# Kernel optimization log

Measured on AMD Instinct MI355X. Metric: run time of the kernel, lower is better.

Reference implementation:

```python
import jax, jax.numpy as jnp
import numpy as np

B, Q, K, D, H = 8, 128, 1024, 256, 256


def setup_inputs() -> dict:
    key = jax.random.key(0)
    ks = jax.random.split(key, 7)
    queries = jax.random.normal(ks[0], (B, Q, D), dtype=jnp.float32)
    keys = jax.random.normal(ks[1], (B, K, D), dtype=jnp.float32)
    values = jax.random.normal(ks[2], (B, K, D), dtype=jnp.float32)
    W_q = jax.random.normal(ks[3], (H, D), dtype=jnp.float32) * (1.0 / np.sqrt(D))
    W_k = jax.random.normal(ks[4], (H, D), dtype=jnp.float32) * (1.0 / np.sqrt(D))
    w_v = jax.random.normal(ks[5], (H,), dtype=jnp.float32) * (1.0 / np.sqrt(H))
    valid_lens = jax.random.randint(ks[6], (B,), 0, K, dtype=jnp.int64)
    return {"queries": queries, "keys": keys, "values": values,
            "W_q": W_q, "W_k": W_k, "w_v": w_v, "valid_lens": valid_lens}


def reference(queries, keys, values, W_q, W_k, w_v, valid_lens):
    # Linear projections (bias=False): [B,Q,H], [B,K,H]
    q = jnp.einsum("bqd,hd->bqh", queries, W_q)
    k = jnp.einsum("bkd,hd->bkh", keys, W_k)
    # Broadcast add -> tanh -> reduce with w_v: scores [B,Q,K]
    features = jnp.tanh(q[:, :, None, :] + k[:, None, :, :])  # [B,Q,K,H]
    scores = jnp.einsum("bqkh,h->bqk", features, w_v)
    # Masked softmax over K: positions >= valid_len get -1e9
    mask = jnp.arange(K)[None, None, :] < valid_lens[:, None, None]
    scores = jnp.where(mask, scores, jnp.float32(-1e9))
    attn = jax.nn.softmax(scores, axis=-1)  # [B,Q,K]
    # Dropout p=0.0 (eval): identity. bmm(attn, values) -> [B,Q,Dv]
    return jnp.einsum("bqk,bkv->bqv", attn, values)
```

## Files before the change

kernel.cpp:

```cpp
#include <hip/hip_runtime.h>

#define BB 8
#define QQ 128
#define KK 1024
#define DD 256
#define HH 256

#define KSPLIT 8
#define KCH (KK / KSPLIT)
#define QT 8

#define TWO_LOG2E     2.8853900817779268f
#define NEG_TWO_LOG2E -2.8853900817779268f

__global__ __launch_bounds__(256) void proj_kernel(const float* __restrict__ queries,
                                                   const float* __restrict__ keys,
                                                   const float* __restrict__ Wq,
                                                   const float* __restrict__ Wk,
                                                   float* __restrict__ eproj) {
    __shared__ float As[64][68];
    __shared__ float Ws[64][68];
    const int t  = threadIdx.x;
    const int tr = t & 15;
    const int th = t >> 4;
    const int r0 = blockIdx.x * 64;
    const int h0 = blockIdx.y * 64;
    const bool isQ = (r0 < BB * QQ);
    const float* A = isQ ? (queries + (size_t)r0 * DD)
                         : (keys + (size_t)(r0 - BB * QQ) * DD);
    const float* W = isQ ? Wq : Wk;

    float acc[4][4] = {};

    for (int dc = 0; dc < DD; dc += 64) {
#pragma unroll
        for (int i = 0; i < 4; ++i) {
            int fi  = t + 256 * i;
            int row = fi >> 4;
            int c4  = (fi & 15) << 2;
            *(float4*)&As[row][c4] = *(const float4*)&A[(size_t)row * DD + dc + c4];
            *(float4*)&Ws[row][c4] = *(const float4*)&W[(size_t)(h0 + row) * DD + dc + c4];
        }
        __syncthreads();
#pragma unroll 4
        for (int dd = 0; dd < 64; dd += 4) {
            float4 a4[4], w4[4];
#pragma unroll
            for (int i = 0; i < 4; ++i) a4[i] = *(float4*)&As[tr + 16 * i][dd];
#pragma unroll
            for (int i = 0; i < 4; ++i) w4[i] = *(float4*)&Ws[th + 16 * i][dd];
#pragma unroll
            for (int ri = 0; ri < 4; ++ri)
#pragma unroll
                for (int hi = 0; hi < 4; ++hi) {
                    acc[ri][hi] += a4[ri].x * w4[hi].x + a4[ri].y * w4[hi].y +
                                   a4[ri].z * w4[hi].z + a4[ri].w * w4[hi].w;
                }
        }
        __syncthreads();
    }
#pragma unroll
    for (int ri = 0; ri < 4; ++ri)
#pragma unroll
        for (int hi = 0; hi < 4; ++hi) {
            eproj[(size_t)(r0 + tr + 16 * ri) * HH + h0 + th + 16 * hi] =
                __builtin_amdgcn_exp2f(TWO_LOG2E * acc[ri][hi]);
        }
}

__global__ __launch_bounds__(256) void score_kernel(const float* __restrict__ eproj,
                                                    const float* __restrict__ wv,
                                                    const int* __restrict__ vlen,
                                                    float* __restrict__ p) {
    __shared__ float qs[32][68];
    __shared__ float ks_[64][68];
    const int t  = threadIdx.x;
    const int tk = t & 15;
    const int tq = t >> 4;
    const int b  = blockIdx.z;
    const int q0 = blockIdx.y * 32;
    const int k0 = blockIdx.x * 64;

    const float* qpB = eproj + ((size_t)(b * QQ + q0)) * HH;
    const float* kpB = eproj + ((size_t)(BB * QQ + b * KK + k0)) * HH;

    float acc[2][4] = {};

    for (int hc = 0; hc < HH; hc += 64) {
#pragma unroll
        for (int i = 0; i < 2; ++i) {
            int fi = t + 256 * i; int row = fi >> 4; int c4 = (fi & 15) << 2;
            *(float4*)&qs[row][c4] = *(const float4*)&qpB[(size_t)row * HH + hc + c4];
        }
#pragma unroll
        for (int i = 0; i < 4; ++i) {
            int fi = t + 256 * i; int row = fi >> 4; int c4 = (fi & 15) << 2;
            *(float4*)&ks_[row][c4] = *(const float4*)&kpB[(size_t)row * HH + hc + c4];
        }
        __syncthreads();

#pragma unroll 4
        for (int hh = 0; hh < 64; hh += 4) {
            const float4 w4 = *(const float4*)&wv[hc + hh];
            const float* wa = (const float*)&w4;
            float4 q4[2], k4[4];
            q4[0] = *(float4*)&qs[tq][hh];
            q4[1] = *(float4*)&qs[tq + 16][hh];
#pragma unroll
            for (int j = 0; j < 4; ++j) k4[j] = *(float4*)&ks_[tk + 16 * j][hh];
#pragma unroll
            for (int i = 0; i < 2; ++i) {
                const float* qa = (const float*)&q4[i];
#pragma unroll
                for (int j = 0; j < 4; ++j) {
                    const float* ka = (const float*)&k4[j];
#pragma unroll
                    for (int cc = 0; cc < 4; ++cc) {
                        float d = __builtin_fmaf(qa[cc], ka[cc], 1.0f);
                        acc[i][j] += wa[cc] * __builtin_amdgcn_rcpf(d);
                    }
                }
            }
        }
        __syncthreads();
    }

    const int vl = vlen[b];
#pragma unroll
    for (int i = 0; i < 2; ++i)
#pragma unroll
        for (int j = 0; j < 4; ++j) {
            int q = q0 + tq + 16 * i;
            int k = k0 + tk + 16 * j;
            float pv;
            if (vl == 0) pv = 1.0f;
            else pv = (k < vl) ? __builtin_amdgcn_exp2f(NEG_TWO_LOG2E * acc[i][j])
                               : 0.0f;
            p[((size_t)b * QQ + q) * KK + k] = pv;
        }
}

__global__ __launch_bounds__(256) void av_partial(const float* __restrict__ p,
                                                  const float* __restrict__ V,
                                                  float* __restrict__ partial,
                                                  float* __restrict__ psum) {
    __shared__ float a_s[QT][KCH];
    const int t   = threadIdx.x;
    const int ksb = blockIdx.x;
    const int q0  = blockIdx.y * QT;
    const int b   = blockIdx.z;
    const int kc0 = ksb * KCH;

    const float* pB = p + ((size_t)b * QQ + q0) * KK + kc0;
    const float* VB = V + ((size_t)b * KK + kc0) * DD;

    {
        int qi = t >> 5;
        int k4 = (t & 31) << 2;
        *(float4*)&a_s[qi][k4] = *(const float4*)&pB[(size_t)qi * KK + k4];
    }
    __syncthreads();

    if (t < QT) {
        float s = 0.f;
        for (int x = 0; x < KCH; x += 4) {
            float4 v = *(float4*)&a_s[t][x];
            s += v.x + v.y + v.z + v.w;
        }
        psum[((size_t)ksb * BB + b) * QQ + q0 + t] = s;
    }

    float acc[QT] = {};
    float vc[8], vn[8];
#pragma unroll
    for (int j = 0; j < 8; ++j) vc[j] = VB[(size_t)j * DD + t];

    for (int kg = 0; kg < KCH; kg += 8) {
        if (kg + 8 < KCH) {
#pragma unroll
            for (int j = 0; j < 8; ++j) vn[j] = VB[(size_t)(kg + 8 + j) * DD + t];
        }
#pragma unroll
        for (int qi = 0; qi < QT; ++qi) {
            float4 a0 = *(float4*)&a_s[qi][kg];
            float4 a1 = *(float4*)&a_s[qi][kg + 4];
            acc[qi] += a0.x * vc[0] + a0.y * vc[1] + a0.z * vc[2] + a0.w * vc[3] +
                       a1.x * vc[4] + a1.y * vc[5] + a1.z * vc[6] + a1.w * vc[7];
        }
#pragma unroll
        for (int j = 0; j < 8; ++j) vc[j] = vn[j];
    }

#pragma unroll
    for (int qi = 0; qi < QT; ++qi) {
        partial[(size_t)ksb * (BB * QQ * DD) +
                ((size_t)b * QQ + q0 + qi) * DD + t] = acc[qi];
    }
}

__global__ __launch_bounds__(256) void av_reduce(const float* __restrict__ partial,
                                                 const float* __restrict__ psum,
                                                 float* __restrict__ out) {
    const int i  = blockIdx.x * 256 + threadIdx.x;
    const int bq = i >> 6;

    float S = 0.f;
#pragma unroll
    for (int ks = 0; ks < KSPLIT; ++ks) S += psum[(size_t)ks * (BB * QQ) + bq];

    const float4* p4 = (const float4*)partial;
    const int stride4 = BB * QQ * DD / 4;
    float4 s = p4[i];
#pragma unroll
    for (int ks = 1; ks < KSPLIT; ++ks) {
        float4 x = p4[(size_t)ks * stride4 + i];
        s.x += x.x; s.y += x.y; s.z += x.z; s.w += x.w;
    }
    const float inv = 1.0f / S;
    s.x *= inv; s.y *= inv; s.z *= inv; s.w *= inv;
    ((float4*)out)[i] = s;
}

extern "C" void kernel_launch(void* const* d_in, const int* in_sizes, int n_in,
                              void* d_out, int out_size, void* d_ws, size_t ws_size,
                              hipStream_t stream) {
    const float* queries = (const float*)d_in[0];
    const float* keys    = (const float*)d_in[1];
    const float* values  = (const float*)d_in[2];
    const float* W_q     = (const float*)d_in[3];
    const float* W_k     = (const float*)d_in[4];
    const float* w_v     = (const float*)d_in[5];
    const int*   vlen    = (const int*)d_in[6];
    float* out = (float*)d_out;

    float* ws    = (float*)d_ws;
    float* eproj = ws;
    float* p     = ws + (size_t)(BB * QQ + BB * KK) * HH;
    float* psum  = p + (size_t)BB * QQ * KK;
    float* partial = ws;

    proj_kernel<<<dim3((BB * QQ + BB * KK) / 64, HH / 64, 1), 256, 0, stream>>>(
        queries, keys, W_q, W_k, eproj);

    score_kernel<<<dim3(KK / 64, QQ / 32, BB), 256, 0, stream>>>(eproj, w_v, vlen, p);

    av_partial<<<dim3(KSPLIT, QQ / QT, BB), 256, 0, stream>>>(p, values, partial, psum);

    av_reduce<<<dim3(BB * QQ * DD / 4 / 256, 1, 1), 256, 0, stream>>>(partial, psum, out);
}
```

Measured before the change: 156.6 us.

## Fuse score and AV kernels, skip masked key tiles in projection and scoring

The score and attention-times-values kernels become one kernel: each block computes a 32x64 tile of unnormalized probabilities, stores it transposed in shared memory, reduces row sums with shuffles and multiplies straight into V. This removes the global round trip of the probability matrix. Key projection blocks and score tiles that lie entirely beyond valid_len are skipped, and skipped score tiles write zero partials. The K split rises to 16 chunks of 64, which doubles the partial-sum traffic that the reduce kernel must read.

Result: faster. 146.2 us (-6.7%).

```diff
diff --git a/kernel.cpp b/kernel.cpp
--- a/kernel.cpp
+++ b/kernel.cpp
@@ -6,9 +6,8 @@
 #define DD 256
 #define HH 256
 
-#define KSPLIT 8
-#define KCH (KK / KSPLIT)
-#define QT 8
+#define KSP 16
+#define KCH 64
 
 #define TWO_LOG2E     2.8853900817779268f
 #define NEG_TWO_LOG2E -2.8853900817779268f
@@ -17,15 +16,23 @@
                                                    const float* __restrict__ keys,
                                                    const float* __restrict__ Wq,
                                                    const float* __restrict__ Wk,
+                                                   const int* __restrict__ vlen,
                                                    float* __restrict__ eproj) {
+    const int r0 = blockIdx.x * 64;
+    const bool isQ = (r0 < BB * QQ);
+    if (!isQ) {
+        const int kb = (r0 - BB * QQ) >> 6;
+        const int b  = kb >> 4;
+        const int k0 = (kb & 15) << 6;
+        if (k0 >= vlen[b]) return;
+    }
+
     __shared__ float As[64][68];
     __shared__ float Ws[64][68];
     const int t  = threadIdx.x;
     const int tr = t & 15;
     const int th = t >> 4;
-    const int r0 = blockIdx.x * 64;
     const int h0 = blockIdx.y * 64;
-    const bool isQ = (r0 < BB * QQ);
     const float* A = isQ ? (queries + (size_t)r0 * DD)
                          : (keys + (size_t)(r0 - BB * QQ) * DD);
     const float* W = isQ ? Wq : Wk;
@@ -68,133 +75,128 @@
         }
 }
 
-__global__ __launch_bounds__(256) void score_kernel(const float* __restrict__ eproj,
-                                                    const float* __restrict__ wv,
-                                                    const int* __restrict__ vlen,
-                                                    float* __restrict__ p) {
+__global__ __launch_bounds__(256) void scoreav_kernel(const float* __restrict__ eproj,
+                                                      const float* __restrict__ wv,
+                                                      const int* __restrict__ vlen,
+                                                      const float* __restrict__ V,
+                                                      float* __restrict__ partial,
+                                                      float* __restrict__ psum) {
     __shared__ float qs[32][68];
     __shared__ float ks_[64][68];
-    const int t  = threadIdx.x;
-    const int tk = t & 15;
-    const int tq = t >> 4;
-    const int b  = blockIdx.z;
-    const int q0 = blockIdx.y * 32;
-    const int k0 = blockIdx.x * 64;
-
-    const float* qpB = eproj + ((size_t)(b * QQ + q0)) * HH;
-    const float* kpB = eproj + ((size_t)(BB * QQ + b * KK + k0)) * HH;
+    __shared__ float pT[KCH][36];
+    const int t   = threadIdx.x;
+    const int tk  = t & 15;
+    const int tq  = t >> 4;
+    const int ksb = blockIdx.x;
+    const int q0  = blockIdx.y * 32;
+    const int b   = blockIdx.z;
+    const int k0  = ksb * KCH;
+    const int vl  = vlen[b];
+
+    const int d4 = (t & 63) << 2;
+    const int qh = (t >> 6) << 3;
+
+    if (vl > 0 && k0 >= vl) {
+        float4 z = {0.f, 0.f, 0.f, 0.f};
+#pragma unroll
+        for (int qi = 0; qi < 8; ++qi) {
+            int q = q0 + qh + qi;
+            *(float4*)&partial[(((size_t)ksb * BB + b) * QQ + q) * DD + d4] = z;
+        }
+        if (t < 32) psum[((size_t)ksb * BB + b) * QQ + q0 + t] = 0.f;
+        return;
+    }
 
     float acc[2][4] = {};
-
-    for (int hc = 0; hc < HH; hc += 64) {
-#pragma unroll
-        for (int i = 0; i < 2; ++i) {
-            int fi = t + 256 * i; int row = fi >> 4; int c4 = (fi & 15) << 2;
-            *(float4*)&qs[row][c4] = *(const float4*)&qpB[(size_t)row * HH + hc + c4];
-        }
-#pragma unroll
-        for (int i = 0; i < 4; ++i) {
-            int fi = t + 256 * i; int row = fi >> 4; int c4 = (fi & 15) << 2;
-            *(float4*)&ks_[row][c4] = *(const float4*)&kpB[(size_t)row * HH + hc + c4];
-        }
-        __syncthreads();
+    if (vl > 0) {
+        const float* qpB = eproj + (size_t)(b * QQ + q0) * HH;
+        const float* kpB = eproj + (size_t)(BB * QQ + b * KK + k0) * HH;
+
+        for (int hc = 0; hc < HH; hc += 64) {
+#pragma unroll
+            for (int i = 0; i < 2; ++i) {
+                int fi = t + 256 * i; int row = fi >> 4; int c4 = (fi & 15) << 2;
+                *(float4*)&qs[row][c4] = *(const float4*)&qpB[(size_t)row * HH + hc + c4];
+            }
+#pragma unroll
+            for (int i = 0; i < 4; ++i) {
+                int fi = t + 256 * i; int row = fi >> 4; int c4 = (fi & 15) << 2;
+                *(float4*)&ks_[row][c4] = *(const float4*)&kpB[(size_t)row * HH + hc + c4];
+            }
+            __syncthreads();
 
 #pragma unroll 4
-        for (int hh = 0; hh < 64; hh += 4) {
-            const float4 w4 = *(const float4*)&wv[hc + hh];
-            const float* wa = (const float*)&w4;
-            float4 q4[2], k4[4];
-            q4[0] = *(float4*)&qs[tq][hh];
-            q4[1] = *(float4*)&qs[tq + 16][hh];
-#pragma unroll
-            for (int j = 0; j < 4; ++j) k4[j] = *(float4*)&ks_[tk + 16 * j][hh];
-#pragma unroll
-            for (int i = 0; i < 2; ++i) {
-                const float* qa = (const float*)&q4[i];
-#pragma unroll
-                for (int j = 0; j < 4; ++j) {
-                    const float* ka = (const float*)&k4[j];
-#pragma unroll
-                    for (int cc = 0; cc < 4; ++cc) {
-                        float d = __builtin_fmaf(qa[cc], ka[cc], 1.0f);
-                        acc[i][j] += wa[cc] * __builtin_amdgcn_rcpf(d);
+            for (int hh = 0; hh < 64; hh += 4) {
+                const float4 w4 = *(const float4*)&wv[hc + hh];
+                const float* wa = (const float*)&w4;
+                float4 q4[2], k4[4];
+                q4[0] = *(float4*)&qs[tq][hh];
+                q4[1] = *(float4*)&qs[tq + 16][hh];
+#pragma unroll
+                for (int j = 0; j < 4; ++j) k4[j] = *(float4*)&ks_[tk + 16 * j][hh];
+#pragma unroll
+                for (int i = 0; i < 2; ++i) {
+                    const float* qa = (const float*)&q4[i];
+#pragma unroll
+                    for (int j = 0; j < 4; ++j) {
+                        const float* ka = (const float*)&k4[j];
+#pragma unroll
+                        for (int cc = 0; cc < 4; ++cc) {
+                            float d = __builtin_fmaf(qa[cc], ka[cc], 1.0f);
+                            acc[i][j] += wa[cc] * __builtin_amdgcn_rcpf(d);
+                        }
                     }
                 }
             }
-        }
-        __syncthreads();
-    }
-
-    const int vl = vlen[b];
+            __syncthreads();
+        }
+    }
+
+    float sj[2] = {0.f, 0.f};
 #pragma unroll
     for (int i = 0; i < 2; ++i)
 #pragma unroll
         for (int j = 0; j < 4; ++j) {
-            int q = q0 + tq + 16 * i;
-            int k = k0 + tk + 16 * j;
+            int kg = k0 + tk + 16 * j;
             float pv;
             if (vl == 0) pv = 1.0f;
-            else pv = (k < vl) ? __builtin_amdgcn_exp2f(NEG_TWO_LOG2E * acc[i][j])
-                               : 0.0f;
-            p[((size_t)b * QQ + q) * KK + k] = pv;
-        }
-}
-
-__global__ __launch_bounds__(256) void av_partial(const float* __restrict__ p,
-                                                  const float* __restrict__ V,
-                                                  float* __restrict__ partial,
-                                                  float* __restrict__ psum) {
-    __shared__ float a_s[QT][KCH];
-    const int t   = threadIdx.x;
-    const int ksb = blockIdx.x;
-    const int q0  = blockIdx.y * QT;
-    const int b   = blockIdx.z;
-    const int kc0 = ksb * KCH;
-
-    const float* pB = p + ((size_t)b * QQ + q0) * KK + kc0;
-    const float* VB = V + ((size_t)b * KK + kc0) * DD;
-
-    {
-        int qi = t >> 5;
-        int k4 = (t & 31) << 2;
-        *(float4*)&a_s[qi][k4] = *(const float4*)&pB[(size_t)qi * KK + k4];
+            else pv = (kg < vl) ? __builtin_amdgcn_exp2f(NEG_TWO_LOG2E * acc[i][j])
+                                : 0.0f;
+            pT[tk + 16 * j][tq + 16 * i] = pv;
+            sj[i] += pv;
+        }
+#pragma unroll
+    for (int off = 1; off < 16; off <<= 1) {
+        sj[0] += __shfl_xor(sj[0], off);
+        sj[1] += __shfl_xor(sj[1], off);
+    }
+    if (tk == 0) {
+        psum[((size_t)ksb * BB + b) * QQ + q0 + tq]      = sj[0];
+        psum[((size_t)ksb * BB + b) * QQ + q0 + tq + 16] = sj[1];
     }
     __syncthreads();
 
-    if (t < QT) {
-        float s = 0.f;
-        for (int x = 0; x < KCH; x += 4) {
-            float4 v = *(float4*)&a_s[t][x];
-            s += v.x + v.y + v.z + v.w;
-        }
-        psum[((size_t)ksb * BB + b) * QQ + q0 + t] = s;
-    }
-
-    float acc[QT] = {};
-    float vc[8], vn[8];
-#pragma unroll
-    for (int j = 0; j < 8; ++j) vc[j] = VB[(size_t)j * DD + t];
-
-    for (int kg = 0; kg < KCH; kg += 8) {
-        if (kg + 8 < KCH) {
-#pragma unroll
-            for (int j = 0; j < 8; ++j) vn[j] = VB[(size_t)(kg + 8 + j) * DD + t];
-        }
-#pragma unroll
-        for (int qi = 0; qi < QT; ++qi) {
-            float4 a0 = *(float4*)&a_s[qi][kg];
-            float4 a1 = *(float4*)&a_s[qi][kg + 4];
-            acc[qi] += a0.x * vc[0] + a0.y * vc[1] + a0.z * vc[2] + a0.w * vc[3] +
-                       a1.x * vc[4] + a1.y * vc[5] + a1.z * vc[6] + a1.w * vc[7];
-        }
-#pragma unroll
-        for (int j = 0; j < 8; ++j) vc[j] = vn[j];
-    }
-
-#pragma unroll
-    for (int qi = 0; qi < QT; ++qi) {
-        partial[(size_t)ksb * (BB * QQ * DD) +
-                ((size_t)b * QQ + q0 + qi) * DD + t] = acc[qi];
+    const float* VB = V + ((size_t)b * KK + k0) * DD;
+    float4 acc4[8] = {};
+#pragma unroll 4
+    for (int k = 0; k < KCH; ++k) {
+        float4 v4 = *(const float4*)&VB[(size_t)k * DD + d4];
+        float4 p0 = *(float4*)&pT[k][qh];
+        float4 p1 = *(float4*)&pT[k][qh + 4];
+        acc4[0].x += p0.x * v4.x; acc4[0].y += p0.x * v4.y; acc4[0].z += p0.x * v4.z; acc4[0].w += p0.x * v4.w;
+        acc4[1].x += p0.y * v4.x; acc4[1].y += p0.y * v4.y; acc4[1].z += p0.y * v4.z; acc4[1].w += p0.y * v4.w;
+        acc4[2].x += p0.z * v4.x; acc4[2].y += p0.z * v4.y; acc4[2].z += p0.z * v4.z; acc4[2].w += p0.z * v4.w;
+        acc4[3].x += p0.w * v4.x; acc4[3].y += p0.w * v4.y; acc4[3].z += p0.w * v4.z; acc4[3].w += p0.w * v4.w;
+        acc4[4].x += p1.x * v4.x; acc4[4].y += p1.x * v4.y; acc4[4].z += p1.x * v4.z; acc4[4].w += p1.x * v4.w;
+        acc4[5].x += p1.y * v4.x; acc4[5].y += p1.y * v4.y; acc4[5].z += p1.y * v4.z; acc4[5].w += p1.y * v4.w;
+        acc4[6].x += p1.z * v4.x; acc4[6].y += p1.z * v4.y; acc4[6].z += p1.z * v4.z; acc4[6].w += p1.z * v4.w;
+        acc4[7].x += p1.w * v4.x; acc4[7].y += p1.w * v4.y; acc4[7].z += p1.w * v4.z; acc4[7].w += p1.w * v4.w;
+    }
+
+#pragma unroll
+    for (int qi = 0; qi < 8; ++qi) {
+        int q = q0 + qh + qi;
+        *(float4*)&partial[(((size_t)ksb * BB + b) * QQ + q) * DD + d4] = acc4[qi];
     }
 }
 
@@ -206,13 +208,13 @@
 
     float S = 0.f;
 #pragma unroll
-    for (int ks = 0; ks < KSPLIT; ++ks) S += psum[(size_t)ks * (BB * QQ) + bq];
+    for (int ks = 0; ks < KSP; ++ks) S += psum[(size_t)ks * (BB * QQ) + bq];
 
     const float4* p4 = (const float4*)partial;
     const int stride4 = BB * QQ * DD / 4;
     float4 s = p4[i];
 #pragma unroll
-    for (int ks = 1; ks < KSPLIT; ++ks) {
+    for (int ks = 1; ks < KSP; ++ks) {
         float4 x = p4[(size_t)ks * stride4 + i];
         s.x += x.x; s.y += x.y; s.z += x.z; s.w += x.w;
     }
@@ -233,18 +235,16 @@
     const int*   vlen    = (const int*)d_in[6];
     float* out = (float*)d_out;
 
-    float* ws    = (float*)d_ws;
-    float* eproj = ws;
-    float* p     = ws + (size_t)(BB * QQ + BB * KK) * HH;
-    float* psum  = p + (size_t)BB * QQ * KK;
-    float* partial = ws;
+    float* ws      = (float*)d_ws;
+    float* eproj   = ws;
+    float* psum    = eproj + (size_t)(BB * QQ + BB * KK) * HH;
+    float* partial = psum + (size_t)KSP * BB * QQ;
 
     proj_kernel<<<dim3((BB * QQ + BB * KK) / 64, HH / 64, 1), 256, 0, stream>>>(
-        queries, keys, W_q, W_k, eproj);
-
-    score_kernel<<<dim3(KK / 64, QQ / 32, BB), 256, 0, stream>>>(eproj, w_v, vlen, p);
-
-    av_partial<<<dim3(KSPLIT, QQ / QT, BB), 256, 0, stream>>>(p, values, partial, psum);
+        queries, keys, W_q, W_k, vlen, eproj);
+
+    scoreav_kernel<<<dim3(KSP, QQ / 32, BB), 256, 0, stream>>>(
+        eproj, w_v, vlen, values, partial, psum);
 
     av_reduce<<<dim3(BB * QQ * DD / 4 / 256, 1, 1), 256, 0, stream>>>(partial, psum, out);
 }
```
